# Kernel tuning notes

Hardware: AMD Instinct MI355X
Metric: run time of the kernel (lower is better)

The kernel has to match this reference:

```python
import jax, jax.numpy as jnp
import numpy as np

LN_EPS = 1e-5
B, T, D, H, NB, HH = 256, 128, 512, 1024, 64, 8


def _layernorm(x, g, b):
    m = x.mean(-1, keepdims=True)
    v = ((x - m) ** 2).mean(-1, keepdims=True)
    return (x - m) / jnp.sqrt(v + LN_EPS) * g + b


def setup_inputs() -> dict:
    key = jax.random.key(0)
    ks = jax.random.split(key, 10)
    init = lambda k, shape, fan: jax.random.normal(k, shape, jnp.float32) * np.float32(1.0 / np.sqrt(fan))
    return {
        "context_features": jax.random.normal(ks[0], (B, T, D), jnp.float32),
        "beam_history": jax.random.randint(ks[1], (B, HH), 0, NB),
        "beam_embed": init(ks[2], (NB, D), D),
        "W_in": init(ks[3], (H, 2 * D), 2 * D), "b_in": jnp.zeros((H,), jnp.float32),
        "W_init": init(ks[4], (H, 2 * D), 2 * D), "b_init": jnp.zeros((H,), jnp.float32),
        "W_ih": init(ks[5], (3 * H, H), H), "b_ih": jnp.zeros((3 * H,), jnp.float32),
        "W_hh": init(ks[6], (3 * H, H), H), "b_hh": jnp.zeros((3 * H,), jnp.float32),
        "ln_g": jnp.ones((H,), jnp.float32), "ln_b": jnp.zeros((H,), jnp.float32),
        "W_o1": init(ks[7], (H, H + D), H + D), "b_o1": jnp.zeros((H,), jnp.float32),
        "W_o2": init(ks[8], (NB, H), H), "b_o2": jnp.zeros((NB,), jnp.float32),
    }


def reference(context_features, beam_history, beam_embed, W_in, b_in, W_init, b_init,
              W_ih, b_ih, W_hh, b_hh, ln_g, ln_b, W_o1, b_o1, W_o2, b_o2):
    # --- init: history embedding mean + global context mean -> initial GRU state ---
    prev0 = beam_history[:, -1]                      # (B,)
    hist_emb = beam_embed[beam_history].mean(axis=1)  # (B, D)
    ctx_global = context_features.mean(axis=1)        # (B, D)
    h0 = jnp.tanh(jnp.concatenate([ctx_global, hist_emb], axis=-1) @ W_init.T + b_init)  # (B, H)

    def step(carry, ctx_t):
        h, prev = carry
        prev_emb = beam_embed[prev]                                            # (B, D)
        x = jax.nn.relu(jnp.concatenate([ctx_t, prev_emb], -1) @ W_in.T + b_in)  # (B, H)
        # PyTorch GRUCell: gate order r, z, n
        gx = x @ W_ih.T + b_ih
        gh = h @ W_hh.T + b_hh
        xr, xz, xn = jnp.split(gx, 3, axis=-1)
        hr, hz, hn = jnp.split(gh, 3, axis=-1)
        r = jax.nn.sigmoid(xr + hr)
        z = jax.nn.sigmoid(xz + hz)
        n = jnp.tanh(xn + r * hn)
        h_new = (1.0 - z) * n + z * h
        h_norm = _layernorm(h_new, ln_g, ln_b)
        o = jax.nn.relu(jnp.concatenate([h_norm, ctx_t], -1) @ W_o1.T + b_o1)
        logits_t = o @ W_o2.T + b_o2                                            # (B, NB)
        pred_next = jnp.argmax(logits_t, axis=-1)
        return (h_new, pred_next), logits_t

    ctx_tbd = jnp.swapaxes(context_features, 0, 1)  # (T, B, D)
    (_, _), logits = jax.lax.scan(step, (h0, prev0), ctx_tbd)
    return jnp.swapaxes(logits, 0, 1)  # (B, T, NB) == ar_logits
```

## Files before the change

kernel.cpp:

```cpp
#include <hip/hip_runtime.h>
#include <hip/hip_bf16.h>


#define TS 68
#define LDPA 40
constexpr int SZ = 262144;
constexpr int TT = 128;
constexpr int LDA_CTX = 65536;

typedef __attribute__((ext_vector_type(8))) short short8_t;
typedef __attribute__((ext_vector_type(4))) float f32x4;


__device__ __forceinline__ unsigned short f2bf_rne(float v) {
    unsigned u = __float_as_uint(v);
    unsigned r = u + 0x7fffu + ((u >> 16) & 1u);
    return (unsigned short)(r >> 16);
}
__device__ __forceinline__ float bfbits2f(unsigned short h) {
    return __uint_as_float(((unsigned)h) << 16);
}
__device__ __forceinline__ void split2(float v, unsigned short& h, unsigned short& l) {
    h = f2bf_rne(v);
    l = f2bf_rne(v - bfbits2f(h));
}
__device__ __forceinline__ void splitA8(const float4& v0, const float4& v1,
                                        short8_t& hi, short8_t& lo) {
    unsigned short h[8], l[8];
    split2(v0.x, h[0], l[0]); split2(v0.y, h[1], l[1]);
    split2(v0.z, h[2], l[2]); split2(v0.w, h[3], l[3]);
    split2(v1.x, h[4], l[4]); split2(v1.y, h[5], l[5]);
    split2(v1.z, h[6], l[6]); split2(v1.w, h[7], l[7]);
    hi = short8_t{(short)h[0],(short)h[1],(short)h[2],(short)h[3],
                  (short)h[4],(short)h[5],(short)h[6],(short)h[7]};
    lo = short8_t{(short)l[0],(short)l[1],(short)l[2],(short)l[3],
                  (short)l[4],(short)l[5],(short)l[6],(short)l[7]};
}


__device__ __forceinline__ void core12b(
    const unsigned short* __restrict__ Ah, const unsigned short* __restrict__ Al,
    int lda, int b0,
    const unsigned short* __restrict__ Bh, int ldb,
    const unsigned short* __restrict__ BlP, int nKs, int ksbase, int nfb,
    int nIter, unsigned short* sm, f32x4 acc[2][4])
{
    const int tid = threadIdx.x, lane = tid & 63, wid = tid >> 6;
    const int wr = wid >> 1, wc = wid & 1;
    const int l15 = lane & 15, kg = (lane >> 4) * 8;
    const int arow = tid >> 2, acol = (tid & 3) * 8;
    const int brow = tid >> 1, bcol = (tid & 1) * 16;

    const int ALO = 2560, BHI = 5120, BUF = 10240;

    const unsigned short* gAh = Ah + (size_t)(b0 + arow) * lda + ksbase * 32 + acol;
    const unsigned short* gAl = Al + (size_t)(b0 + arow) * lda + ksbase * 32 + acol;
    const unsigned short* gBh = Bh + (size_t)brow * ldb + ksbase * 32 + bcol;
    const unsigned short* pBl[4];
#pragma unroll
    for (int ni = 0; ni < 4; ++ni)
        pBl[ni] = BlP + ((size_t)(nfb + ni) * nKs + ksbase) * 512 + lane * 8;

    short8_t cBl[4], nBl[4];
    {
        short8_t a_h = *(const short8_t*)gAh;
        short8_t a_l = *(const short8_t*)gAl;
        short8_t b0h = *(const short8_t*)gBh;
        short8_t b1h = *(const short8_t*)(gBh + 8);
        *(short8_t*)&sm[arow * LDPA + acol]            = a_h;
        *(short8_t*)&sm[ALO + arow * LDPA + acol]      = a_l;
        *(short8_t*)&sm[BHI + brow * LDPA + bcol]      = b0h;
        *(short8_t*)&sm[BHI + brow * LDPA + bcol + 8]  = b1h;
#pragma unroll
        for (int ni = 0; ni < 4; ++ni) cBl[ni] = *(const short8_t*)pBl[ni];
    }
    __syncthreads();

    int cur = 0;
    const int aro = (wr * 32 + l15) * LDPA + kg;
    for (int i = 0; i < nIter; ++i) {
        short8_t a_h, a_l, b0h, b1h;
        if (i + 1 < nIter) {
            const int ko = (i + 1) * 32;
            a_h = *(const short8_t*)(gAh + ko);
            a_l = *(const short8_t*)(gAl + ko);
            b0h = *(const short8_t*)(gBh + ko);
            b1h = *(const short8_t*)(gBh + ko + 8);
#pragma unroll
            for (int ni = 0; ni < 4; ++ni)
                nBl[ni] = *(const short8_t*)(pBl[ni] + (size_t)(i + 1) * 512);
        }
        const unsigned short* S = sm + cur * BUF;
        short8_t afh[2], afl[2];
#pragma unroll
        for (int mi = 0; mi < 2; ++mi) {
            afh[mi] = *(const short8_t*)&S[aro + mi * 16 * LDPA];
            afl[mi] = *(const short8_t*)&S[ALO + aro + mi * 16 * LDPA];
        }
#pragma unroll
        for (int ni = 0; ni < 4; ++ni) {
            short8_t b_h = *(const short8_t*)&S[BHI + (wc * 64 + ni * 16 + l15) * LDPA + kg];
#pragma unroll
            for (int mi = 0; mi < 2; ++mi) {
                acc[mi][ni] = __builtin_amdgcn_mfma_f32_16x16x32_bf16(afh[mi], b_h, acc[mi][ni], 0, 0, 0);
                acc[mi][ni] = __builtin_amdgcn_mfma_f32_16x16x32_bf16(afh[mi], cBl[ni], acc[mi][ni], 0, 0, 0);
                acc[mi][ni] = __builtin_amdgcn_mfma_f32_16x16x32_bf16(afl[mi], b_h, acc[mi][ni], 0, 0, 0);
            }
        }
        if (i + 1 < nIter) {
            unsigned short* N_ = sm + (cur ^ 1) * BUF;
            *(short8_t*)&N_[arow * LDPA + acol]           = a_h;
            *(short8_t*)&N_[ALO + arow * LDPA + acol]     = a_l;
            *(short8_t*)&N_[BHI + brow * LDPA + bcol]     = b0h;
            *(short8_t*)&N_[BHI + brow * LDPA + bcol + 8] = b1h;
        }
        __syncthreads();
        cur ^= 1;
#pragma unroll
        for (int ni = 0; ni < 4; ++ni) cBl[ni] = nBl[ni];
    }
}


__device__ __forceinline__ void mfma_core9(
    const float* __restrict__ A, int lda, int b0,
    const unsigned short* __restrict__ Bh, const unsigned short* __restrict__ Bl,
    int ldb, int n0, int k0base, int nIter,
    unsigned short* sm, f32x4 acc[2][4])
{
    const int tid = threadIdx.x, lane = tid & 63, wid = tid >> 6;
    const int wr = wid >> 1, wc = wid & 1;
    const int l15 = lane & 15, kg = (lane >> 4) * 8;
    const int arow = tid >> 2, acol = (tid & 3) * 8;
    const int brow = tid >> 1, bcol = (tid & 1) * 16;

    const int AOFF = 2560, BHOFF = 5120, BLOFF = 10240, BUF = 15360;

    const float* gA = A + (size_t)(b0 + arow) * lda + k0base + acol;
    const unsigned short* gBh = Bh + (size_t)(n0 + brow) * ldb + k0base + bcol;
    const unsigned short* gBl = Bl + (size_t)(n0 + brow) * ldb + k0base + bcol;

    {
        float4 a0 = *(const float4*)gA;
        float4 a1 = *(const float4*)(gA + 4);
        short8_t ah, al;
        splitA8(a0, a1, ah, al);
        short8_t bh0 = *(const short8_t*)gBh;
        short8_t bh1 = *(const short8_t*)(gBh + 8);
        short8_t bl0 = *(const short8_t*)gBl;
        short8_t bl1 = *(const short8_t*)(gBl + 8);
        *(short8_t*)&sm[arow * LDPA + acol]              = ah;
        *(short8_t*)&sm[AOFF + arow * LDPA + acol]       = al;
        *(short8_t*)&sm[BHOFF + brow * LDPA + bcol]      = bh0;
        *(short8_t*)&sm[BHOFF + brow * LDPA + bcol + 8]  = bh1;
        *(short8_t*)&sm[BLOFF + brow * LDPA + bcol]      = bl0;
        *(short8_t*)&sm[BLOFF + brow * LDPA + bcol + 8]  = bl1;
    }
    __syncthreads();

    int cur = 0;
    const int aro = (wr * 32 + l15) * LDPA + kg;
    for (int i = 0; i < nIter; ++i) {
        float4 a0, a1;
        short8_t bh0, bh1, bl0, bl1;
        if (i + 1 < nIter) {
            const int ko = (i + 1) * 32;
            a0 = *(const float4*)(gA + ko);
            a1 = *(const float4*)(gA + ko + 4);
            bh0 = *(const short8_t*)(gBh + ko);
            bh1 = *(const short8_t*)(gBh + ko + 8);
            bl0 = *(const short8_t*)(gBl + ko);
            bl1 = *(const short8_t*)(gBl + ko + 8);
        }
        const unsigned short* S = sm + cur * BUF;
        short8_t afh[2], afl[2];
#pragma unroll
        for (int mi = 0; mi < 2; ++mi) {
            afh[mi] = *(const short8_t*)&S[aro + mi * 16 * LDPA];
            afl[mi] = *(const short8_t*)&S[AOFF + aro + mi * 16 * LDPA];
        }
#pragma unroll
        for (int ni = 0; ni < 4; ++ni) {
            const int bro = (wc * 64 + ni * 16 + l15) * LDPA + kg;
            short8_t b_h = *(const short8_t*)&S[BHOFF + bro];
            short8_t b_l = *(const short8_t*)&S[BLOFF + bro];
#pragma unroll
            for (int mi = 0; mi < 2; ++mi) {
                acc[mi][ni] = __builtin_amdgcn_mfma_f32_16x16x32_bf16(afh[mi], b_h, acc[mi][ni], 0, 0, 0);
                acc[mi][ni] = __builtin_amdgcn_mfma_f32_16x16x32_bf16(afh[mi], b_l, acc[mi][ni], 0, 0, 0);
                acc[mi][ni] = __builtin_amdgcn_mfma_f32_16x16x32_bf16(afl[mi], b_h, acc[mi][ni], 0, 0, 0);
            }
        }
        if (i + 1 < nIter) {
            short8_t ah, al;
            splitA8(a0, a1, ah, al);
            unsigned short* N_ = sm + (cur ^ 1) * BUF;
            *(short8_t*)&N_[arow * LDPA + acol]             = ah;
            *(short8_t*)&N_[AOFF + arow * LDPA + acol]      = al;
            *(short8_t*)&N_[BHOFF + brow * LDPA + bcol]     = bh0;
            *(short8_t*)&N_[BHOFF + brow * LDPA + bcol + 8] = bh1;
            *(short8_t*)&N_[BLOFF + brow * LDPA + bcol]     = bl0;
            *(short8_t*)&N_[BLOFF + brow * LDPA + bcol + 8] = bl1;
        }
        __syncthreads();
        cur ^= 1;
    }
}


__device__ __forceinline__ void gemm_tile64(
    const float* __restrict__ A, int lda, int Mlim, int b0,
    const float* __restrict__ W, int ldw, int n0, int K,
    float* At, float* Wt, float acc[4][4])
{
    const int tid = threadIdx.x;
    const int tx = tid & 15, ty = tid >> 4;
    const int r = tid >> 2, c0 = (tid & 3) << 2;
    for (int k0 = 0; k0 < K; k0 += 16) {
        float4 av = make_float4(0.f, 0.f, 0.f, 0.f);
        if (b0 + r < Mlim)
            av = *(const float4*)(A + (size_t)(b0 + r) * lda + k0 + c0);
        float4 wv = *(const float4*)(W + (size_t)(n0 + r) * ldw + k0 + c0);
        __syncthreads();
        At[(c0+0)*TS + r] = av.x; At[(c0+1)*TS + r] = av.y;
        At[(c0+2)*TS + r] = av.z; At[(c0+3)*TS + r] = av.w;
        Wt[(c0+0)*TS + r] = wv.x; Wt[(c0+1)*TS + r] = wv.y;
        Wt[(c0+2)*TS + r] = wv.z; Wt[(c0+3)*TS + r] = wv.w;
        __syncthreads();
#pragma unroll
        for (int kk = 0; kk < 16; ++kk) {
            float4 a = *(const float4*)(At + kk*TS + ty*4);
            float4 w = *(const float4*)(Wt + kk*TS + tx*4);
            acc[0][0] += a.x*w.x; acc[0][1] += a.x*w.y; acc[0][2] += a.x*w.z; acc[0][3] += a.x*w.w;
            acc[1][0] += a.y*w.x; acc[1][1] += a.y*w.y; acc[1][2] += a.y*w.z; acc[1][3] += a.y*w.w;
            acc[2][0] += a.z*w.x; acc[2][1] += a.z*w.y; acc[2][2] += a.z*w.z; acc[2][3] += a.z*w.w;
            acc[3][0] += a.w*w.x; acc[3][1] += a.w*w.y; acc[3][2] += a.w*w.z; acc[3][3] += a.w*w.w;
        }
    }
}


__global__ void pre0_kernel(const float* __restrict__ ctx, const int* __restrict__ bh,
                            const float* __restrict__ be, float* __restrict__ A0,
                            int* __restrict__ prev)
{
    int b = blockIdx.x, tid = threadIdx.x;
    float s = 0.f;
    for (int t = 0; t < TT; ++t) s += ctx[(size_t)b * LDA_CTX + t * 512 + tid];
    A0[b * 1024 + tid] = s * (1.f / 128.f);
    float s2 = 0.f;
    for (int i = 0; i < 8; ++i) s2 += be[bh[b * 8 + i] * 512 + tid];
    A0[b * 1024 + 512 + tid] = s2 * 0.125f;
    if (tid == 0) prev[b] = bh[b * 8 + 7];
}

__global__ void wo2t_kernel(const float* __restrict__ W_o2, float* __restrict__ Wo2t)
{
    int idx = blockIdx.x * 256 + threadIdx.x;
    int k = idx >> 6, n = idx & 63;
    Wo2t[idx] = W_o2[n * 1024 + k];
}

__global__ void uv_kernel(const float* __restrict__ ln_g, const float* __restrict__ ln_b,
                          const float* __restrict__ W_o1, float* __restrict__ uvv)
{
    int idx = blockIdx.x * 256 + threadIdx.x;
    int which = idx >> 10, j = idx & 1023;
    const float* vec = which ? ln_b : ln_g;
    float s = 0.f;
    for (int k = 0; k < 1024; ++k) s += vec[k] * W_o1[(size_t)j * 1536 + k];
    uvv[which * 1024 + j] = s;
}

__global__ void whi_kernel(const float* __restrict__ src, int ld, int col0,
                           int N, int K, const float* __restrict__ scale,
                           unsigned short* __restrict__ hi)
{
    int idx = blockIdx.x * 256 + threadIdx.x;
    if (idx >= N * K) return;
    int n = idx / K, k = idx - n * K;
    float v = src[(size_t)n * ld + col0 + k];
    if (scale) v *= scale[k];
    hi[idx] = f2bf_rne(v);
}

__global__ void packlo_kernel(const float* __restrict__ src, int ld, int col0,
                              int N, int K, const float* __restrict__ scale,
                              unsigned short* __restrict__ lo)
{
    int idx = blockIdx.x * 256 + threadIdx.x;
    if (idx >= N * K) return;
    int j = idx & 7;
    int lane = (idx >> 3) & 63;
    int fs = idx >> 9;
    int nKs = K >> 5;
    int nf = fs / nKs, ks = fs - nf * nKs;
    int n = nf * 16 + (lane & 15);
    int k = ks * 32 + (lane >> 4) * 8 + j;
    float v = src[(size_t)n * ld + col0 + k];
    if (scale) v *= scale[k];
    unsigned short h, l;
    split2(v, h, l);
    lo[idx] = l;
}

__global__ void wsplit_kernel(const float* __restrict__ src, int src_ld, int col0,
                              int N, int K, const float* __restrict__ scale,
                              unsigned short* __restrict__ hi,
                              unsigned short* __restrict__ lo)
{
    int idx = blockIdx.x * 256 + threadIdx.x;
    if (idx >= N * K) return;
    int n = idx / K, k = idx - n * K;
    float v = src[(size_t)n * src_ld + col0 + k];
    if (scale) v *= scale[k];
    unsigned short h, l;
    split2(v, h, l);
    hi[idx] = h; lo[idx] = l;
}

__global__ void gemm64_kernel(const float* __restrict__ A, int lda, int M,
                              const float* __restrict__ W, int ldw, int K,
                              const float* __restrict__ bias,
                              float* __restrict__ C, int ldc, int act)
{
    __shared__ __align__(16) float At[16 * TS];
    __shared__ __align__(16) float Wt[16 * TS];
    float acc[4][4] = {};
    int b0 = blockIdx.x * 64, n0 = blockIdx.y * 64;
    gemm_tile64(A, lda, M, b0, W, ldw, n0, K, At, Wt, acc);
    int tx = threadIdx.x & 15, ty = threadIdx.x >> 4;
#pragma unroll
    for (int i = 0; i < 4; ++i) {
        int b = b0 + ty * 4 + i;
        if (b >= M) continue;
#pragma unroll
        for (int j = 0; j < 4; ++j) {
            int n = n0 + tx * 4 + j;
            float v = acc[i][j] + (bias ? bias[n] : 0.f);
            if (act == 1) v = tanhf(v);
            C[(size_t)b * ldc + n] = v;
        }
    }
}

__global__ void xbuild0s_kernel(const float* __restrict__ cin0, const float* __restrict__ bpart,
                                const int* __restrict__ prev,
                                unsigned short* __restrict__ xh, unsigned short* __restrict__ xl)
{
    int b = blockIdx.x, tid = threadIdx.x;
    int pb = prev[b];
#pragma unroll
    for (int jj = 0; jj < 4; ++jj) {
        int j = jj * 256 + tid;
        float v = fmaxf(cin0[(size_t)b * 1024 + j] + bpart[(size_t)pb * 1024 + j], 0.f);
        unsigned short h, l;
        split2(v, h, l);
        xh[(size_t)b * 1024 + j] = h;
        xl[(size_t)b * 1024 + j] = l;
    }
}

__global__ void xbuild0_kernel(const float* __restrict__ cin0, const float* __restrict__ bpart,
                               const int* __restrict__ prev, float* __restrict__ x)
{
    int b = blockIdx.x, tid = threadIdx.x;
    int pb = prev[b];
#pragma unroll
    for (int jj = 0; jj < 4; ++jj) {
        int j = jj * 256 + tid;
        x[(size_t)b * 1024 + j] = fmaxf(cin0[(size_t)b * 1024 + j] + bpart[(size_t)pb * 1024 + j], 0.f);
    }
}


__global__ __launch_bounds__(256) void gates12_kernel(
    const unsigned short* __restrict__ xh, const unsigned short* __restrict__ xl,
    const unsigned short* __restrict__ hh, const unsigned short* __restrict__ hl,
    const float* __restrict__ ctx,
    const unsigned short* __restrict__ wih_hi, const unsigned short* __restrict__ wih_loP,
    const unsigned short* __restrict__ whh_hi, const unsigned short* __restrict__ whh_loP,
    const unsigned short* __restrict__ wcin_hi, const unsigned short* __restrict__ wcin_lo,
    const unsigned short* __restrict__ wo1c_hi, const unsigned short* __restrict__ wo1c_lo,
    const float* __restrict__ b_in, const float* __restrict__ b_o1,
    float* __restrict__ g6, float* __restrict__ cin, float* __restrict__ octx,
    int t)
{
    const int bid = blockIdx.x;
    const int z = bid & 7;
    const int tile = bid >> 3;
    const int tm = tile & 3, tn = tile >> 2;
    if (z == 6 && t + 1 >= TT) return;
    const int b0 = tm * 64, n0 = tn * 128;

    __shared__ __align__(16) unsigned short sm[2 * 15360];
    f32x4 acc[2][4] = {};
    const float* bias = nullptr;
    float* C;
    const int wid = threadIdx.x >> 6, wc = wid & 1;

    if (z < 6) {
        int g = z % 3, s = z / 3;
        const unsigned short* Ah = s ? hh : xh;
        const unsigned short* Al = s ? hl : xl;
        const unsigned short* Bh = (s ? whh_hi : wih_hi) + (size_t)(g * 1024 + n0) * 1024;
        const unsigned short* BlP = s ? whh_loP : wih_loP;
        const int nfb = g * 64 + (n0 >> 4) + wc * 4;
        C = g6 + (size_t)z * SZ;
        core12b(Ah, Al, 1024, b0, Bh, 1024, BlP, 32, 0, nfb, 32, sm, acc);
    } else if (z == 6) {
        const float* A = ctx + (size_t)(t + 1) * 512;
        bias = b_in; C = cin;
        mfma_core9(A, LDA_CTX, b0, wcin_hi, wcin_lo, 512, n0, 0, 16, sm, acc);
    } else {
        const float* A = ctx + (size_t)t * 512;
        bias = b_o1; C = octx;
        mfma_core9(A, LDA_CTX, b0, wo1c_hi, wo1c_lo, 512, n0, 0, 16, sm, acc);
    }

    const int lane = threadIdx.x & 63;
    const int wr = wid >> 1;
    const int l15 = lane & 15, g4 = (lane >> 4) * 4;
#pragma unroll
    for (int mi = 0; mi < 2; ++mi) {
#pragma unroll
        for (int ni = 0; ni < 4; ++ni) {
            int col = n0 + wc * 64 + ni * 16 + l15;
            float bv = bias ? bias[col] : 0.f;
#pragma unroll
            for (int r = 0; r < 4; ++r) {
                int row = b0 + wr * 32 + mi * 16 + g4 + r;
                C[(size_t)row * 1024 + col] = acc[mi][ni][r] + bv;
            }
        }
    }
}

__global__ __launch_bounds__(256) void kb12_kernel(
    const unsigned short* __restrict__ hh, const unsigned short* __restrict__ hl,
    const unsigned short* __restrict__ wo1k_hi, const unsigned short* __restrict__ wo1k_loP,
    float* __restrict__ g6)
{
    const int bid = blockIdx.x;
    const int tm = bid >> 5, tn = (bid >> 2) & 7, p = bid & 3;
    const int b0 = tm * 64, n0 = tn * 128;
    const int wid = threadIdx.x >> 6, wc = wid & 1;

    __shared__ __align__(16) unsigned short sm[2 * 10240];
    f32x4 acc[2][4] = {};
    core12b(hh, hl, 1024, b0, wo1k_hi + (size_t)n0 * 1024, 1024,
            wo1k_loP, 32, p * 8, (n0 >> 4) + wc * 4, 8, sm, acc);

    float* C = g6 + (size_t)p * SZ;
    const int lane = threadIdx.x & 63;
    const int wr = wid >> 1;
    const int l15 = lane & 15, g4 = (lane >> 4) * 4;
#pragma unroll
    for (int mi = 0; mi < 2; ++mi) {
#pragma unroll
        for (int ni = 0; ni < 4; ++ni) {
            int col = n0 + wc * 64 + ni * 16 + l15;
#pragma unroll
            for (int r = 0; r < 4; ++r) {
                int row = b0 + wr * 32 + mi * 16 + g4 + r;
                C[(size_t)row * 1024 + col] = acc[mi][ni][r];
            }
        }
    }
}

__global__ void gru_ln6_kernel(const float* __restrict__ g6,
                               const float* __restrict__ b_ih, const float* __restrict__ b_hh,
                               float* __restrict__ h,
                               unsigned short* __restrict__ hh, unsigned short* __restrict__ hl,
                               float* __restrict__ mbuf, float* __restrict__ isbuf)
{
    __shared__ float ls[4], lq[4];
    int b = blockIdx.x, tid = threadIdx.x;
    float s = 0.f, q = 0.f;
#pragma unroll
    for (int jj = 0; jj < 4; ++jj) {
        int j = jj * 256 + tid;
        size_t base = (size_t)b * 1024 + j;
        float xr = g6[0 * (size_t)SZ + base] + b_ih[j];
        float xz = g6[1 * (size_t)SZ + base] + b_ih[1024 + j];
        float xn = g6[2 * (size_t)SZ + base] + b_ih[2048 + j];
        float hr = g6[3 * (size_t)SZ + base] + b_hh[j];
        float hz = g6[4 * (size_t)SZ + base] + b_hh[1024 + j];
        float hn = g6[5 * (size_t)SZ + base] + b_hh[2048 + j];
        float r = 1.f / (1.f + expf(-(xr + hr)));
        float z = 1.f / (1.f + expf(-(xz + hz)));
        float nn = tanhf(xn + r * hn);
        float ho = h[base];
        float hv = (1.f - z) * nn + z * ho;
        h[base] = hv;
        unsigned short a, c;
        split2(hv, a, c); hh[base] = a; hl[base] = c;
        s += hv; q += hv * hv;
    }
    for (int off = 32; off; off >>= 1) {
        s += __shfl_down(s, off);
        q += __shfl_down(q, off);
    }
    int lane = tid & 63, w = tid >> 6;
    if (lane == 0) { ls[w] = s; lq[w] = q; }
    __syncthreads();
    if (tid == 0) {
        float S = ls[0] + ls[1] + ls[2] + ls[3];
        float Q = lq[0] + lq[1] + lq[2] + lq[3];
        float m = S * (1.f / 1024.f);
        mbuf[b] = m;
        isbuf[b] = rsqrtf(Q * (1.f / 1024.f) - m * m + 1e-5f);
    }
}

__global__ void kc12_kernel(const float* __restrict__ g6,
                            const float* __restrict__ Wo2t, const float* __restrict__ b_o2,
                            const float* __restrict__ uv, const float* __restrict__ octx,
                            const float* __restrict__ mbuf, const float* __restrict__ isbuf,
                            const float* __restrict__ cin, const float* __restrict__ bpart,
                            unsigned short* __restrict__ xh, unsigned short* __restrict__ xl,
                            int* __restrict__ prev, float* __restrict__ out, int t)
{
    __shared__ __align__(16) float os[4][1024];
    __shared__ float red[4][4][64];
    __shared__ int sidx[4];
    const int b0 = blockIdx.x * 4, tid = threadIdx.x;

#pragma unroll
    for (int i = 0; i < 4; ++i) {
        int f = tid + i * 256;
        int r = f >> 8, c4 = (f & 255) << 2;
        size_t base = (size_t)(b0 + r) * 1024 + c4;
        float4 p0 = *(const float4*)(g6 + base);
        float4 p1 = *(const float4*)(g6 + (size_t)SZ + base);
        float4 p2 = *(const float4*)(g6 + 2 * (size_t)SZ + base);
        float4 p3 = *(const float4*)(g6 + 3 * (size_t)SZ + base);
        float4 oc = *(const float4*)(octx + base);
        float4 u4 = *(const float4*)(uv + c4);
        float4 v4 = *(const float4*)(uv + 1024 + c4);
        float m = mbuf[b0 + r], is = isbuf[b0 + r];
        float4 o4;
        o4.x = fmaxf((p0.x + p1.x + p2.x + p3.x - m * u4.x) * is + v4.x + oc.x, 0.f);
        o4.y = fmaxf((p0.y + p1.y + p2.y + p3.y - m * u4.y) * is + v4.y + oc.y, 0.f);
        o4.z = fmaxf((p0.z + p1.z + p2.z + p3.z - m * u4.z) * is + v4.z + oc.z, 0.f);
        o4.w = fmaxf((p0.w + p1.w + p2.w + p3.w - m * u4.w) * is + v4.w + oc.w, 0.f);
        *(float4*)&os[r][c4] = o4;
    }
    __syncthreads();

    {
        int n = tid & 63, seg = tid >> 6;
        float p0 = 0.f, p1 = 0.f, p2 = 0.f, p3 = 0.f;
        int k0 = seg * 256;
        for (int k = k0; k < k0 + 256; ++k) {
            float w = Wo2t[(size_t)k * 64 + n];
            p0 += os[0][k] * w; p1 += os[1][k] * w;
            p2 += os[2][k] * w; p3 += os[3][k] * w;
        }
        red[0][seg][n] = p0; red[1][seg][n] = p1;
        red[2][seg][n] = p2; red[3][seg][n] = p3;
    }
    __syncthreads();

    {
        int r = tid >> 6, n = tid & 63;
        float lg = red[r][0][n] + red[r][1][n] + red[r][2][n] + red[r][3][n] + b_o2[n];
        out[(size_t)(b0 + r) * (TT * 64) + t * 64 + n] = lg;
        float v = lg; int idx = n;
        for (int off = 32; off; off >>= 1) {
            float ov = __shfl_xor(v, off);
            int oi = __shfl_xor(idx, off);
            if (ov > v || (ov == v && oi < idx)) { v = ov; idx = oi; }
        }
        if (n == 0) { prev[b0 + r] = idx; sidx[r] = idx; }
    }
    __syncthreads();

    if (t + 1 < TT) {
#pragma unroll
        for (int i = 0; i < 16; ++i) {
            int idx = tid + i * 256;
            int r = idx >> 10, j = idx & 1023;
            float v = fmaxf(cin[(size_t)(b0 + r) * 1024 + j] +
                            bpart[(size_t)sidx[r] * 1024 + j], 0.f);
            unsigned short h, l;
            split2(v, h, l);
            xh[(size_t)(b0 + r) * 1024 + j] = h;
            xl[(size_t)(b0 + r) * 1024 + j] = l;
        }
    }
}


__global__ void step_gemms_kernel(
    const float* __restrict__ x, const float* __restrict__ hBase,
    const float* __restrict__ ctx,
    const float* __restrict__ Wih, const float* __restrict__ Whh,
    const float* __restrict__ Win, const float* __restrict__ Wo1,
    const float* __restrict__ b_in, const float* __restrict__ b_o1,
    float* __restrict__ g6, float* __restrict__ cinBase, float* __restrict__ octx,
    int t)
{
    __shared__ __align__(16) float At[16 * TS];
    __shared__ __align__(16) float Wt[16 * TS];
    float acc[4][4] = {};
    const int z = blockIdx.z, b0 = blockIdx.x * 64, n0 = blockIdx.y * 64;
    const float *A, *W, *bias = nullptr;
    float* C;
    int lda, ldw, K;
    if (z < 6) {
        int g = z % 3, s = z / 3;
        A = s ? (hBase + (size_t)(t & 1) * SZ) : x;
        lda = 1024;
        W = (s ? Whh : Wih) + (size_t)(g * 1024) * 1024;
        ldw = 1024; K = 1024;
        C = g6 + (size_t)z * SZ;
    } else if (z == 6) {
        if (t + 1 >= TT) return;
        A = ctx + (size_t)(t + 1) * 512; lda = LDA_CTX;
        W = Win; ldw = 1024; K = 512; bias = b_in;
        C = cinBase + (size_t)((t + 1) & 1) * SZ;
    } else {
        A = ctx + (size_t)t * 512; lda = LDA_CTX;
        W = Wo1 + 1024; ldw = 1536; K = 512; bias = b_o1;
        C = octx;
    }
    gemm_tile64(A, lda, 256, b0, W, ldw, n0, K, At, Wt, acc);
    int tx = threadIdx.x & 15, ty = threadIdx.x >> 4;
#pragma unroll
    for (int i = 0; i < 4; ++i) {
        int b = b0 + ty * 4 + i;
#pragma unroll
        for (int j = 0; j < 4; ++j) {
            int n = n0 + tx * 4 + j;
            float v = acc[i][j];
            if (bias) v += bias[n];
            C[(size_t)b * 1024 + n] = v;
        }
    }
}

__global__ void kb_kernel(const float* __restrict__ hg, const float* __restrict__ Wo1,
                          const float* __restrict__ uv, const float* __restrict__ octx,
                          const float* __restrict__ mbuf, const float* __restrict__ isbuf,
                          float* __restrict__ o)
{
    __shared__ __align__(16) float At[16 * TS];
    __shared__ __align__(16) float Wt[16 * TS];
    float acc[2][4] = {};
    const int b0 = blockIdx.x * 32, n0 = blockIdx.y * 64;
    const int tid = threadIdx.x, tx = tid & 15, ty = tid >> 4;
    const int r = tid >> 2, c0 = (tid & 3) << 2;
    for (int k0 = 0; k0 < 1024; k0 += 16) {
        float4 av = make_float4(0.f, 0.f, 0.f, 0.f);
        if (r < 32) av = *(const float4*)(hg + (size_t)(b0 + r) * 1024 + k0 + c0);
        float4 wv = *(const float4*)(Wo1 + (size_t)(n0 + r) * 1536 + k0 + c0);
        __syncthreads();
        At[(c0+0)*TS + r] = av.x; At[(c0+1)*TS + r] = av.y;
        At[(c0+2)*TS + r] = av.z; At[(c0+3)*TS + r] = av.w;
        Wt[(c0+0)*TS + r] = wv.x; Wt[(c0+1)*TS + r] = wv.y;
        Wt[(c0+2)*TS + r] = wv.z; Wt[(c0+3)*TS + r] = wv.w;
        __syncthreads();
#pragma unroll
        for (int kk = 0; kk < 16; ++kk) {
            float2 a = *(const float2*)(At + kk*TS + ty*2);
            float4 w = *(const float4*)(Wt + kk*TS + tx*4);
            acc[0][0] += a.x*w.x; acc[0][1] += a.x*w.y; acc[0][2] += a.x*w.z; acc[0][3] += a.x*w.w;
            acc[1][0] += a.y*w.x; acc[1][1] += a.y*w.y; acc[1][2] += a.y*w.z; acc[1][3] += a.y*w.w;
        }
    }
#pragma unroll
    for (int i = 0; i < 2; ++i) {
        int b = b0 + ty * 2 + i;
        float m = mbuf[b], is = isbuf[b];
#pragma unroll
        for (int j = 0; j < 4; ++j) {
            int n = n0 + tx * 4 + j;
            float v = (acc[i][j] - m * uv[n]) * is + uv[1024 + n] + octx[(size_t)b * 1024 + n];
            o[(size_t)b * 1024 + n] = fmaxf(v, 0.f);
        }
    }
}

__global__ void gru_ln_kernel(const float* __restrict__ g6,
                              const float* __restrict__ b_ih, const float* __restrict__ b_hh,
                              float* __restrict__ hBase, const float* __restrict__ ln_g,
                              float* __restrict__ hg, float* __restrict__ mbuf,
                              float* __restrict__ isbuf, int t)
{
    __shared__ float rs[256], rq[256];
    int b = blockIdx.x, tid = threadIdx.x;
    const float* hc = hBase + (size_t)(t & 1) * SZ + (size_t)b * 1024;
    float* hnx = hBase + (size_t)((t + 1) & 1) * SZ + (size_t)b * 1024;
    float s = 0.f, q = 0.f;
#pragma unroll
    for (int jj = 0; jj < 4; ++jj) {
        int j = jj * 256 + tid;
        size_t base = (size_t)b * 1024 + j;
        float xr = g6[0 * (size_t)SZ + base] + b_ih[j];
        float xz = g6[1 * (size_t)SZ + base] + b_ih[1024 + j];
        float xn = g6[2 * (size_t)SZ + base] + b_ih[2048 + j];
        float hr = g6[3 * (size_t)SZ + base] + b_hh[j];
        float hz = g6[4 * (size_t)SZ + base] + b_hh[1024 + j];
        float hn = g6[5 * (size_t)SZ + base] + b_hh[2048 + j];
        float r = 1.f / (1.f + expf(-(xr + hr)));
        float z = 1.f / (1.f + expf(-(xz + hz)));
        float nn = tanhf(xn + r * hn);
        float ho = hc[j];
        float hv = (1.f - z) * nn + z * ho;
        hnx[j] = hv;
        hg[base] = hv * ln_g[j];
        s += hv; q += hv * hv;
    }
    rs[tid] = s; rq[tid] = q;
    __syncthreads();
    for (int st = 128; st; st >>= 1) {
        if (tid < st) { rs[tid] += rs[tid + st]; rq[tid] += rq[tid + st]; }
        __syncthreads();
    }
    if (tid == 0) {
        float m = rs[0] * (1.f / 1024.f);
        float var = rq[0] * (1.f / 1024.f) - m * m;
        mbuf[b] = m;
        isbuf[b] = rsqrtf(var + 1e-5f);
    }
}

__global__ void kc_kernel(const float* __restrict__ o, const float* __restrict__ Wo2t,
                          const float* __restrict__ b_o2, const float* __restrict__ cinBase,
                          const float* __restrict__ bpart, float* __restrict__ x,
                          int* __restrict__ prev, float* __restrict__ out, int t)
{
    __shared__ __align__(16) float os[1024];
    __shared__ float red[4][64];
    __shared__ int sidx;
    int b = blockIdx.x, tid = threadIdx.x;
    const float* orow = o + (size_t)b * 1024;
    *(float4*)&os[tid * 4] = *(const float4*)&orow[tid * 4];
    __syncthreads();
    int n = tid & 63, seg = tid >> 6;
    float p = 0.f;
    int k0 = seg * 256;
#pragma unroll 8
    for (int k = 0; k < 256; ++k) p += os[k0 + k] * Wo2t[(size_t)(k0 + k) * 64 + n];
    red[seg][n] = p;
    __syncthreads();
    if (tid < 64) {
        float lg = red[0][tid] + red[1][tid] + red[2][tid] + red[3][tid] + b_o2[tid];
        out[((size_t)b * TT + t) * 64 + tid] = lg;
        float v = lg; int idx = tid;
        for (int off = 32; off; off >>= 1) {
            float ov = __shfl_xor(v, off);
            int oi = __shfl_xor(idx, off);
            if (ov > v || (ov == v && oi < idx)) { v = ov; idx = oi; }
        }
        if (tid == 0) { prev[b] = idx; sidx = idx; }
    }
    __syncthreads();
    if (t + 1 < TT) {
        int pb = sidx;
        const float* cn = cinBase + (size_t)((t + 1) & 1) * SZ + (size_t)b * 1024;
        const float* bp = bpart + (size_t)pb * 1024;
#pragma unroll
        for (int jj = 0; jj < 4; ++jj) {
            int j = jj * 256 + tid;
            x[(size_t)b * 1024 + j] = fmaxf(cn[j] + bp[j], 0.f);
        }
    }
}

__global__ void copy_gb_kernel(const float* g, const float* bb, float* gb)
{
    int idx = blockIdx.x * 256 + threadIdx.x;
    if (idx < 1024) gb[idx] = g[idx];
    else            gb[idx] = bb[idx - 1024];
}


extern "C" void kernel_launch(void* const* d_in, const int* in_sizes, int n_in,
                              void* d_out, int out_size, void* d_ws, size_t ws_size,
                              hipStream_t stream)
{
    const float* ctx    = (const float*)d_in[0];
    const int*   bh     = (const int*)d_in[1];
    const float* be     = (const float*)d_in[2];
    const float* W_in   = (const float*)d_in[3];
    const float* b_in   = (const float*)d_in[4];
    const float* W_init = (const float*)d_in[5];
    const float* b_init = (const float*)d_in[6];
    const float* W_ih   = (const float*)d_in[7];
    const float* b_ih   = (const float*)d_in[8];
    const float* W_hh   = (const float*)d_in[9];
    const float* b_hh   = (const float*)d_in[10];
    const float* ln_g   = (const float*)d_in[11];
    const float* ln_b   = (const float*)d_in[12];
    const float* W_o1   = (const float*)d_in[13];
    const float* b_o1   = (const float*)d_in[14];
    const float* W_o2   = (const float*)d_in[15];
    const float* b_o2   = (const float*)d_in[16];
    float* out = (float*)d_out;
    float* ws  = (float*)d_ws;

    const bool mfma_path = (ws_size >= 45700000ull);

    if (mfma_path) {
        float* hbuf  = ws;
        float* cin   = ws + 262144;
        float* octx  = ws + 524288;
        float* g6    = ws + 786432;
        float* A0    = g6;
        float* bpart = ws + 2359296;
        float* uvv   = ws + 2424832;
        float* Wo2t  = ws + 2428928;
        float* mbuf  = ws + 2494464;
        float* isbuf = ws + 2494720;
        int*   prev  = (int*)(ws + 2494976);
        unsigned short* bf = (unsigned short*)(ws + 2495232);
        unsigned short* wih_hi   = bf;
        unsigned short* wih_loP  = bf + 3145728;
        unsigned short* whh_hi   = bf + 6291456;
        unsigned short* whh_loP  = bf + 9437184;
        unsigned short* wo1k_hi  = bf + 12582912;
        unsigned short* wo1k_loP = bf + 13631488;
        unsigned short* wo1c_hi  = bf + 14680064;
        unsigned short* wo1c_lo  = bf + 15204352;
        unsigned short* wcin_hi  = bf + 15728640;
        unsigned short* wcin_lo  = bf + 16252928;
        unsigned short* xh       = bf + 16777216;
        unsigned short* xl       = bf + 17039360;
        unsigned short* hh       = bf + 17301504;
        unsigned short* hl       = bf + 17563648;

        pre0_kernel<<<256, 512, 0, stream>>>(ctx, bh, be, A0, prev);
        wo2t_kernel<<<256, 256, 0, stream>>>(W_o2, Wo2t);
        uv_kernel<<<8, 256, 0, stream>>>(ln_g, ln_b, W_o1, uvv);
        gemm64_kernel<<<dim3(4, 16), 256, 0, stream>>>(A0, 1024, 256, W_init, 1024, 1024,
                                                       b_init, hbuf, 1024, 1);
        gemm64_kernel<<<dim3(1, 16), 256, 0, stream>>>(be, 512, 64, W_in + 512, 1024, 512,
                                                       nullptr, bpart, 1024, 0);
        gemm64_kernel<<<dim3(4, 16), 256, 0, stream>>>(ctx, LDA_CTX, 256, W_in, 1024, 512,
                                                       b_in, cin, 1024, 0);
        xbuild0s_kernel<<<256, 256, 0, stream>>>(cin, bpart, prev, xh, xl);
        whi_kernel<<<12288, 256, 0, stream>>>(W_ih, 1024, 0, 3072, 1024, nullptr, wih_hi);
        packlo_kernel<<<12288, 256, 0, stream>>>(W_ih, 1024, 0, 3072, 1024, nullptr, wih_loP);
        whi_kernel<<<12288, 256, 0, stream>>>(W_hh, 1024, 0, 3072, 1024, nullptr, whh_hi);
        packlo_kernel<<<12288, 256, 0, stream>>>(W_hh, 1024, 0, 3072, 1024, nullptr, whh_loP);
        whi_kernel<<<4096, 256, 0, stream>>>(W_o1, 1536, 0, 1024, 1024, ln_g, wo1k_hi);
        packlo_kernel<<<4096, 256, 0, stream>>>(W_o1, 1536, 0, 1024, 1024, ln_g, wo1k_loP);
        wsplit_kernel<<<2048, 256, 0, stream>>>(W_o1, 1536, 1024, 1024, 512, nullptr, wo1c_hi, wo1c_lo);
        wsplit_kernel<<<2048, 256, 0, stream>>>(W_in, 1024, 0, 1024, 512, nullptr, wcin_hi, wcin_lo);
        wsplit_kernel<<<1024, 256, 0, stream>>>(hbuf, 1024, 0, 256, 1024, nullptr, hh, hl);

        for (int t = 0; t < TT; ++t) {
            gates12_kernel<<<256, 256, 0, stream>>>(
                xh, xl, hh, hl, ctx,
                wih_hi, wih_loP, whh_hi, whh_loP, wcin_hi, wcin_lo, wo1c_hi, wo1c_lo,
                b_in, b_o1, g6, cin, octx, t);
            gru_ln6_kernel<<<256, 256, 0, stream>>>(g6, b_ih, b_hh, hbuf,
                                                    hh, hl, mbuf, isbuf);
            kb12_kernel<<<128, 256, 0, stream>>>(hh, hl, wo1k_hi, wo1k_loP, g6);
            kc12_kernel<<<64, 256, 0, stream>>>(g6, Wo2t, b_o2, uvv, octx, mbuf, isbuf,
                                                cin, bpart, xh, xl, prev, out, t);
        }
    } else {
        float* A0    = ws;
        float* hbuf  = ws + 262144;
        float* hg    = ws + 786432;
        float* x     = ws + 1048576;
        float* cin   = ws + 1310720;
        float* octx  = ws + 1835008;
        float* g6    = ws + 2097152;
        float* obuf  = ws + 3670016;
        float* bpart = ws + 3932160;
        float* uvv   = ws + 3997696;
        float* gb    = ws + 3999744;
        float* Wo2t  = ws + 4001792;
        float* mbuf  = ws + 4067328;
        float* isbuf = ws + 4067584;
        int*   prev  = (int*)(ws + 4067840);

        pre0_kernel<<<256, 512, 0, stream>>>(ctx, bh, be, A0, prev);
        copy_gb_kernel<<<8, 256, 0, stream>>>(ln_g, ln_b, gb);
        wo2t_kernel<<<256, 256, 0, stream>>>(W_o2, Wo2t);
        gemm64_kernel<<<dim3(4, 16), 256, 0, stream>>>(A0, 1024, 256, W_init, 1024, 1024,
                                                       b_init, hbuf, 1024, 1);
        gemm64_kernel<<<dim3(1, 16), 256, 0, stream>>>(be, 512, 64, W_in + 512, 1024, 512,
                                                       nullptr, bpart, 1024, 0);
        gemm64_kernel<<<dim3(1, 16), 256, 0, stream>>>(gb, 1024, 2, W_o1, 1536, 1024,
                                                       nullptr, uvv, 1024, 0);
        gemm64_kernel<<<dim3(4, 16), 256, 0, stream>>>(ctx, LDA_CTX, 256, W_in, 1024, 512,
                                                       b_in, cin, 1024, 0);
        xbuild0_kernel<<<256, 256, 0, stream>>>(cin, bpart, prev, x);

        for (int t = 0; t < TT; ++t) {
            step_gemms_kernel<<<dim3(4, 16, 8), 256, 0, stream>>>(
                x, hbuf, ctx, W_ih, W_hh, W_in, W_o1, b_in, b_o1, g6, cin, octx, t);
            gru_ln_kernel<<<256, 256, 0, stream>>>(g6, b_ih, b_hh, hbuf, ln_g, hg,
                                                   mbuf, isbuf, t);
            kb_kernel<<<dim3(8, 16), 256, 0, stream>>>(hg, W_o1, uvv, octx, mbuf, isbuf, obuf);
            kc_kernel<<<256, 256, 0, stream>>>(obuf, Wo2t, b_o2, cin, bpart, x, prev, out, t);
        }
    }
}
```

Measured before the change: 7.335 ms.

## Prepack high-part weights into MFMA fragment layout and bypass LDS for B

The bf16 high halves of the GRU and output weights are now pre-packed into the per-lane MFMA fragment order, the same way the low halves already were. The GEMM core then loads B fragments straight from global memory into registers, skipping the LDS staging and LDS reads for B and halving shared memory per block. The GRU elementwise kernel is also vectorised to float4 loads and stores. The cost is more global fragment loads held in registers per iteration, which raises register pressure and gives up LDS reuse of B across the wave rows.

```diff
diff --git a/kernel.cpp b/kernel.cpp
--- a/kernel.cpp
+++ b/kernel.cpp
@@ -38,57 +38,58 @@
 }
 
 
-__device__ __forceinline__ void core12b(
+__device__ __forceinline__ void core13b(
     const unsigned short* __restrict__ Ah, const unsigned short* __restrict__ Al,
     int lda, int b0,
-    const unsigned short* __restrict__ Bh, int ldb,
-    const unsigned short* __restrict__ BlP, int nKs, int ksbase, int nfb,
+    const unsigned short* __restrict__ BhP, const unsigned short* __restrict__ BlP,
+    int nKs, int ksbase, int nfb,
     int nIter, unsigned short* sm, f32x4 acc[2][4])
 {
     const int tid = threadIdx.x, lane = tid & 63, wid = tid >> 6;
     const int wr = wid >> 1, wc = wid & 1;
     const int l15 = lane & 15, kg = (lane >> 4) * 8;
     const int arow = tid >> 2, acol = (tid & 3) * 8;
-    const int brow = tid >> 1, bcol = (tid & 1) * 16;
-
-    const int ALO = 2560, BHI = 5120, BUF = 10240;
+
+    const int ALO = 2560, BUF = 5120;
 
     const unsigned short* gAh = Ah + (size_t)(b0 + arow) * lda + ksbase * 32 + acol;
     const unsigned short* gAl = Al + (size_t)(b0 + arow) * lda + ksbase * 32 + acol;
-    const unsigned short* gBh = Bh + (size_t)brow * ldb + ksbase * 32 + bcol;
+    const unsigned short* pBh[4];
     const unsigned short* pBl[4];
 #pragma unroll
-    for (int ni = 0; ni < 4; ++ni)
+    for (int ni = 0; ni < 4; ++ni) {
+        pBh[ni] = BhP + ((size_t)(nfb + ni) * nKs + ksbase) * 512 + lane * 8;
         pBl[ni] = BlP + ((size_t)(nfb + ni) * nKs + ksbase) * 512 + lane * 8;
-
-    short8_t cBl[4], nBl[4];
+    }
+
+    short8_t cBh[4], cBl[4], nBh[4], nBl[4];
     {
         short8_t a_h = *(const short8_t*)gAh;
         short8_t a_l = *(const short8_t*)gAl;
-        short8_t b0h = *(const short8_t*)gBh;
-        short8_t b1h = *(const short8_t*)(gBh + 8);
-        *(short8_t*)&sm[arow * LDPA + acol]            = a_h;
-        *(short8_t*)&sm[ALO + arow * LDPA + acol]      = a_l;
-        *(short8_t*)&sm[BHI + brow * LDPA + bcol]      = b0h;
-        *(short8_t*)&sm[BHI + brow * LDPA + bcol + 8]  = b1h;
-#pragma unroll
-        for (int ni = 0; ni < 4; ++ni) cBl[ni] = *(const short8_t*)pBl[ni];
+        *(short8_t*)&sm[arow * LDPA + acol]       = a_h;
+        *(short8_t*)&sm[ALO + arow * LDPA + acol] = a_l;
+#pragma unroll
+        for (int ni = 0; ni < 4; ++ni) {
+            cBh[ni] = *(const short8_t*)pBh[ni];
+            cBl[ni] = *(const short8_t*)pBl[ni];
+        }
     }
     __syncthreads();
 
     int cur = 0;
     const int aro = (wr * 32 + l15) * LDPA + kg;
     for (int i = 0; i < nIter; ++i) {
-        short8_t a_h, a_l, b0h, b1h;
+        short8_t a_h, a_l;
         if (i + 1 < nIter) {
             const int ko = (i + 1) * 32;
             a_h = *(const short8_t*)(gAh + ko);
             a_l = *(const short8_t*)(gAl + ko);
-            b0h = *(const short8_t*)(gBh + ko);
-            b1h = *(const short8_t*)(gBh + ko + 8);
-#pragma unroll
-            for (int ni = 0; ni < 4; ++ni)
-                nBl[ni] = *(const short8_t*)(pBl[ni] + (size_t)(i + 1) * 512);
+            const size_t fo = (size_t)(i + 1) * 512;
+#pragma unroll
+            for (int ni = 0; ni < 4; ++ni) {
+                nBh[ni] = *(const short8_t*)(pBh[ni] + fo);
+                nBl[ni] = *(const short8_t*)(pBl[ni] + fo);
+            }
         }
         const unsigned short* S = sm + cur * BUF;
         short8_t afh[2], afl[2];
@@ -99,25 +100,22 @@
         }
 #pragma unroll
         for (int ni = 0; ni < 4; ++ni) {
-            short8_t b_h = *(const short8_t*)&S[BHI + (wc * 64 + ni * 16 + l15) * LDPA + kg];
 #pragma unroll
             for (int mi = 0; mi < 2; ++mi) {
-                acc[mi][ni] = __builtin_amdgcn_mfma_f32_16x16x32_bf16(afh[mi], b_h, acc[mi][ni], 0, 0, 0);
+                acc[mi][ni] = __builtin_amdgcn_mfma_f32_16x16x32_bf16(afh[mi], cBh[ni], acc[mi][ni], 0, 0, 0);
                 acc[mi][ni] = __builtin_amdgcn_mfma_f32_16x16x32_bf16(afh[mi], cBl[ni], acc[mi][ni], 0, 0, 0);
-                acc[mi][ni] = __builtin_amdgcn_mfma_f32_16x16x32_bf16(afl[mi], b_h, acc[mi][ni], 0, 0, 0);
+                acc[mi][ni] = __builtin_amdgcn_mfma_f32_16x16x32_bf16(afl[mi], cBh[ni], acc[mi][ni], 0, 0, 0);
             }
         }
         if (i + 1 < nIter) {
             unsigned short* N_ = sm + (cur ^ 1) * BUF;
-            *(short8_t*)&N_[arow * LDPA + acol]           = a_h;
-            *(short8_t*)&N_[ALO + arow * LDPA + acol]     = a_l;
-            *(short8_t*)&N_[BHI + brow * LDPA + bcol]     = b0h;
-            *(short8_t*)&N_[BHI + brow * LDPA + bcol + 8] = b1h;
+            *(short8_t*)&N_[arow * LDPA + acol]       = a_h;
+            *(short8_t*)&N_[ALO + arow * LDPA + acol] = a_l;
         }
         __syncthreads();
         cur ^= 1;
 #pragma unroll
-        for (int ni = 0; ni < 4; ++ni) cBl[ni] = nBl[ni];
+        for (int ni = 0; ni < 4; ++ni) { cBh[ni] = nBh[ni]; cBl[ni] = nBl[ni]; }
     }
 }
 
@@ -272,13 +270,19 @@
     uvv[which * 1024 + j] = s;
 }
 
-__global__ void whi_kernel(const float* __restrict__ src, int ld, int col0,
-                           int N, int K, const float* __restrict__ scale,
-                           unsigned short* __restrict__ hi)
+__global__ void packhi_kernel(const float* __restrict__ src, int ld, int col0,
+                              int N, int K, const float* __restrict__ scale,
+                              unsigned short* __restrict__ hi)
 {
     int idx = blockIdx.x * 256 + threadIdx.x;
     if (idx >= N * K) return;
-    int n = idx / K, k = idx - n * K;
+    int j = idx & 7;
+    int lane = (idx >> 3) & 63;
+    int fs = idx >> 9;
+    int nKs = K >> 5;
+    int nf = fs / nKs, ks = fs - nf * nKs;
+    int n = nf * 16 + (lane & 15);
+    int k = ks * 32 + (lane >> 4) * 8 + j;
     float v = src[(size_t)n * ld + col0 + k];
     if (scale) v *= scale[k];
     hi[idx] = f2bf_rne(v);
@@ -374,12 +378,12 @@
 }
 
 
-__global__ __launch_bounds__(256) void gates12_kernel(
+__global__ __launch_bounds__(256) void gates13_kernel(
     const unsigned short* __restrict__ xh, const unsigned short* __restrict__ xl,
     const unsigned short* __restrict__ hh, const unsigned short* __restrict__ hl,
     const float* __restrict__ ctx,
-    const unsigned short* __restrict__ wih_hi, const unsigned short* __restrict__ wih_loP,
-    const unsigned short* __restrict__ whh_hi, const unsigned short* __restrict__ whh_loP,
+    const unsigned short* __restrict__ wih_hiP, const unsigned short* __restrict__ wih_loP,
+    const unsigned short* __restrict__ whh_hiP, const unsigned short* __restrict__ whh_loP,
     const unsigned short* __restrict__ wcin_hi, const unsigned short* __restrict__ wcin_lo,
     const unsigned short* __restrict__ wo1c_hi, const unsigned short* __restrict__ wo1c_lo,
     const float* __restrict__ b_in, const float* __restrict__ b_o1,
@@ -403,11 +407,11 @@
         int g = z % 3, s = z / 3;
         const unsigned short* Ah = s ? hh : xh;
         const unsigned short* Al = s ? hl : xl;
-        const unsigned short* Bh = (s ? whh_hi : wih_hi) + (size_t)(g * 1024 + n0) * 1024;
+        const unsigned short* BhP = s ? whh_hiP : wih_hiP;
         const unsigned short* BlP = s ? whh_loP : wih_loP;
         const int nfb = g * 64 + (n0 >> 4) + wc * 4;
         C = g6 + (size_t)z * SZ;
-        core12b(Ah, Al, 1024, b0, Bh, 1024, BlP, 32, 0, nfb, 32, sm, acc);
+        core13b(Ah, Al, 1024, b0, BhP, BlP, 32, 0, nfb, 32, sm, acc);
     } else if (z == 6) {
         const float* A = ctx + (size_t)(t + 1) * 512;
         bias = b_in; C = cin;
@@ -436,9 +440,9 @@
     }
 }
 
-__global__ __launch_bounds__(256) void kb12_kernel(
+__global__ __launch_bounds__(256) void kb13_kernel(
     const unsigned short* __restrict__ hh, const unsigned short* __restrict__ hl,
-    const unsigned short* __restrict__ wo1k_hi, const unsigned short* __restrict__ wo1k_loP,
+    const unsigned short* __restrict__ wo1k_hiP, const unsigned short* __restrict__ wo1k_loP,
     float* __restrict__ g6)
 {
     const int bid = blockIdx.x;
@@ -446,10 +450,10 @@
     const int b0 = tm * 64, n0 = tn * 128;
     const int wid = threadIdx.x >> 6, wc = wid & 1;
 
-    __shared__ __align__(16) unsigned short sm[2 * 10240];
+    __shared__ __align__(16) unsigned short sm[2 * 5120];
     f32x4 acc[2][4] = {};
-    core12b(hh, hl, 1024, b0, wo1k_hi + (size_t)n0 * 1024, 1024,
-            wo1k_loP, 32, p * 8, (n0 >> 4) + wc * 4, 8, sm, acc);
+    core13b(hh, hl, 1024, b0, wo1k_hiP, wo1k_loP, 32, p * 8,
+            (n0 >> 4) + wc * 4, 8, sm, acc);
 
     float* C = g6 + (size_t)p * SZ;
     const int lane = threadIdx.x & 63;
@@ -469,40 +473,67 @@
     }
 }
 
-__global__ void gru_ln6_kernel(const float* __restrict__ g6,
-                               const float* __restrict__ b_ih, const float* __restrict__ b_hh,
-                               float* __restrict__ h,
-                               unsigned short* __restrict__ hh, unsigned short* __restrict__ hl,
-                               float* __restrict__ mbuf, float* __restrict__ isbuf)
+__global__ void gru13_kernel(const float* __restrict__ g6,
+                             const float* __restrict__ b_ih, const float* __restrict__ b_hh,
+                             float* __restrict__ h,
+                             unsigned short* __restrict__ hh, unsigned short* __restrict__ hl,
+                             float* __restrict__ mbuf, float* __restrict__ isbuf)
 {
     __shared__ float ls[4], lq[4];
-    int b = blockIdx.x, tid = threadIdx.x;
-    float s = 0.f, q = 0.f;
-#pragma unroll
-    for (int jj = 0; jj < 4; ++jj) {
-        int j = jj * 256 + tid;
-        size_t base = (size_t)b * 1024 + j;
-        float xr = g6[0 * (size_t)SZ + base] + b_ih[j];
-        float xz = g6[1 * (size_t)SZ + base] + b_ih[1024 + j];
-        float xn = g6[2 * (size_t)SZ + base] + b_ih[2048 + j];
-        float hr = g6[3 * (size_t)SZ + base] + b_hh[j];
-        float hz = g6[4 * (size_t)SZ + base] + b_hh[1024 + j];
-        float hn = g6[5 * (size_t)SZ + base] + b_hh[2048 + j];
-        float r = 1.f / (1.f + expf(-(xr + hr)));
-        float z = 1.f / (1.f + expf(-(xz + hz)));
-        float nn = tanhf(xn + r * hn);
-        float ho = h[base];
-        float hv = (1.f - z) * nn + z * ho;
-        h[base] = hv;
-        unsigned short a, c;
-        split2(hv, a, c); hh[base] = a; hl[base] = c;
-        s += hv; q += hv * hv;
-    }
+    const int b = blockIdx.x, tid = threadIdx.x;
+    const int j = tid * 4;
+    size_t base = (size_t)b * 1024 + j;
+    float4 xr = *(const float4*)(g6 + base);
+    float4 xz = *(const float4*)(g6 + (size_t)SZ + base);
+    float4 xn = *(const float4*)(g6 + 2 * (size_t)SZ + base);
+    float4 hr = *(const float4*)(g6 + 3 * (size_t)SZ + base);
+    float4 hz = *(const float4*)(g6 + 4 * (size_t)SZ + base);
+    float4 hn = *(const float4*)(g6 + 5 * (size_t)SZ + base);
+    float4 ho = *(const float4*)(h + base);
+    float4 bi0 = *(const float4*)(b_ih + j);
+    float4 bi1 = *(const float4*)(b_ih + 1024 + j);
+    float4 bi2 = *(const float4*)(b_ih + 2048 + j);
+    float4 bh0 = *(const float4*)(b_hh + j);
+    float4 bh1 = *(const float4*)(b_hh + 1024 + j);
+    float4 bh2 = *(const float4*)(b_hh + 2048 + j);
+    float4 hv;
+    {
+        float rr = 1.f / (1.f + expf(-((xr.x + bi0.x) + (hr.x + bh0.x))));
+        float zz = 1.f / (1.f + expf(-((xz.x + bi1.x) + (hz.x + bh1.x))));
+        float nn = tanhf((xn.x + bi2.x) + rr * (hn.x + bh2.x));
+        hv.x = (1.f - zz) * nn + zz * ho.x;
+    }
+    {
+        float rr = 1.f / (1.f + expf(-((xr.y + bi0.y) + (hr.y + bh0.y))));
+        float zz = 1.f / (1.f + expf(-((xz.y + bi1.y) + (hz.y + bh1.y))));
+        float nn = tanhf((xn.y + bi2.y) + rr * (hn.y + bh2.y));
+        hv.y = (1.f - zz) * nn + zz * ho.y;
+    }
+    {
+        float rr = 1.f / (1.f + expf(-((xr.z + bi0.z) + (hr.z + bh0.z))));
+        float zz = 1.f / (1.f + expf(-((xz.z + bi1.z) + (hz.z + bh1.z))));
+        float nn = tanhf((xn.z + bi2.z) + rr * (hn.z + bh2.z));
+        hv.z = (1.f - zz) * nn + zz * ho.z;
+    }
+    {
+        float rr = 1.f / (1.f + expf(-((xr.w + bi0.w) + (hr.w + bh0.w))));
+        float zz = 1.f / (1.f + expf(-((xz.w + bi1.w) + (hz.w + bh1.w))));
+        float nn = tanhf((xn.w + bi2.w) + rr * (hn.w + bh2.w));
+        hv.w = (1.f - zz) * nn + zz * ho.w;
+    }
+    *(float4*)(h + base) = hv;
+    ushort4 h4, l4;
+    split2(hv.x, h4.x, l4.x); split2(hv.y, h4.y, l4.y);
+    split2(hv.z, h4.z, l4.z); split2(hv.w, h4.w, l4.w);
+    *(ushort4*)(hh + base) = h4;
+    *(ushort4*)(hl + base) = l4;
+    float s = hv.x + hv.y + hv.z + hv.w;
+    float q = hv.x * hv.x + hv.y * hv.y + hv.z * hv.z + hv.w * hv.w;
     for (int off = 32; off; off >>= 1) {
         s += __shfl_down(s, off);
         q += __shfl_down(q, off);
     }
-    int lane = tid & 63, w = tid >> 6;
+    const int lane = tid & 63, w = tid >> 6;
     if (lane == 0) { ls[w] = s; lq[w] = q; }
     __syncthreads();
     if (tid == 0) {
@@ -514,7 +545,7 @@
     }
 }
 
-__global__ void kc12_kernel(const float* __restrict__ g6,
+__global__ void kc13_kernel(const float* __restrict__ g6,
                             const float* __restrict__ Wo2t, const float* __restrict__ b_o2,
                             const float* __restrict__ uv, const float* __restrict__ octx,
                             const float* __restrict__ mbuf, const float* __restrict__ isbuf,
@@ -817,11 +848,11 @@
         float* isbuf = ws + 2494720;
         int*   prev  = (int*)(ws + 2494976);
         unsigned short* bf = (unsigned short*)(ws + 2495232);
-        unsigned short* wih_hi   = bf;
+        unsigned short* wih_hiP  = bf;
         unsigned short* wih_loP  = bf + 3145728;
-        unsigned short* whh_hi   = bf + 6291456;
+        unsigned short* whh_hiP  = bf + 6291456;
         unsigned short* whh_loP  = bf + 9437184;
-        unsigned short* wo1k_hi  = bf + 12582912;
+        unsigned short* wo1k_hiP = bf + 12582912;
         unsigned short* wo1k_loP = bf + 13631488;
         unsigned short* wo1c_hi  = bf + 14680064;
         unsigned short* wo1c_lo  = bf + 15204352;
@@ -842,25 +873,25 @@
         gemm64_kernel<<<dim3(4, 16), 256, 0, stream>>>(ctx, LDA_CTX, 256, W_in, 1024, 512,
                                                        b_in, cin, 1024, 0);
         xbuild0s_kernel<<<256, 256, 0, stream>>>(cin, bpart, prev, xh, xl);
-        whi_kernel<<<12288, 256, 0, stream>>>(W_ih, 1024, 0, 3072, 1024, nullptr, wih_hi);
+        packhi_kernel<<<12288, 256, 0, stream>>>(W_ih, 1024, 0, 3072, 1024, nullptr, wih_hiP);
         packlo_kernel<<<12288, 256, 0, stream>>>(W_ih, 1024, 0, 3072, 1024, nullptr, wih_loP);
-        whi_kernel<<<12288, 256, 0, stream>>>(W_hh, 1024, 0, 3072, 1024, nullptr, whh_hi);
+        packhi_kernel<<<12288, 256, 0, stream>>>(W_hh, 1024, 0, 3072, 1024, nullptr, whh_hiP);
         packlo_kernel<<<12288, 256, 0, stream>>>(W_hh, 1024, 0, 3072, 1024, nullptr, whh_loP);
-        whi_kernel<<<4096, 256, 0, stream>>>(W_o1, 1536, 0, 1024, 1024, ln_g, wo1k_hi);
+        packhi_kernel<<<4096, 256, 0, stream>>>(W_o1, 1536, 0, 1024, 1024, ln_g, wo1k_hiP);
         packlo_kernel<<<4096, 256, 0, stream>>>(W_o1, 1536, 0, 1024, 1024, ln_g, wo1k_loP);
         wsplit_kernel<<<2048, 256, 0, stream>>>(W_o1, 1536, 1024, 1024, 512, nullptr, wo1c_hi, wo1c_lo);
         wsplit_kernel<<<2048, 256, 0, stream>>>(W_in, 1024, 0, 1024, 512, nullptr, wcin_hi, wcin_lo);
         wsplit_kernel<<<1024, 256, 0, stream>>>(hbuf, 1024, 0, 256, 1024, nullptr, hh, hl);
 
         for (int t = 0; t < TT; ++t) {
-            gates12_kernel<<<256, 256, 0, stream>>>(
+            gates13_kernel<<<256, 256, 0, stream>>>(
                 xh, xl, hh, hl, ctx,
-                wih_hi, wih_loP, whh_hi, whh_loP, wcin_hi, wcin_lo, wo1c_hi, wo1c_lo,
+                wih_hiP, wih_loP, whh_hiP, whh_loP, wcin_hi, wcin_lo, wo1c_hi, wo1c_lo,
                 b_in, b_o1, g6, cin, octx, t);
-            gru_ln6_kernel<<<256, 256, 0, stream>>>(g6, b_ih, b_hh, hbuf,
-                                                    hh, hl, mbuf, isbuf);
-            kb12_kernel<<<128, 256, 0, stream>>>(hh, hl, wo1k_hi, wo1k_loP, g6);
-            kc12_kernel<<<64, 256, 0, stream>>>(g6, Wo2t, b_o2, uvv, octx, mbuf, isbuf,
+            gru13_kernel<<<256, 256, 0, stream>>>(g6, b_ih, b_hh, hbuf,
+                                                  hh, hl, mbuf, isbuf);
+            kb13_kernel<<<128, 256, 0, stream>>>(hh, hl, wo1k_hiP, wo1k_loP, g6);
+            kc13_kernel<<<64, 256, 0, stream>>>(g6, Wo2t, b_o2, uvv, octx, mbuf, isbuf,
                                                 cin, bpart, xh, xl, prev, out, t);
         }
     } else {
```

Result: faster. 6.596 ms (median of 2 runs) (-10.1%).
